# Kernel optimization log

Hardware: AMD Instinct MI355X
Metric: run time of the kernel (lower is better)

The kernel has to match this reference:

```python
import jax, jax.numpy as jnp
import numpy as np

B, S, D = 2, 8192, 1024
H, HD, FD = 16, 64, 256

def setup_inputs() -> dict:
    key = jax.random.key(0)
    ks = jax.random.split(key, 6)
    sc = 1.0 / np.sqrt(D)
    return {
        "hidden_states": jax.random.normal(ks[0], (B, S, D), jnp.float32),
        "Wq": jax.random.normal(ks[1], (D, D), jnp.float32) * sc,
        "Wk": jax.random.normal(ks[2], (D, D), jnp.float32) * sc,
        "Wv": jax.random.normal(ks[3], (D, D), jnp.float32) * sc,
        "Wo": jax.random.normal(ks[4], (D, D), jnp.float32) * sc,
        "Wf": jax.random.normal(ks[5], (FD, HD), jnp.float32) * (1.0 / np.sqrt(HD)),
    }

def reference(hidden_states, Wq, Wk, Wv, Wo, Wf):
    b, s, _ = hidden_states.shape
    # projections (torch Linear: x @ W.T), split heads -> (b, s, h, hd)
    q = (hidden_states @ Wq.T).reshape(b, s, H, HD)
    k = (hidden_states @ Wk.T).reshape(b, s, H, HD)
    v = (hidden_states @ Wv.T).reshape(b, s, H, HD)
    # elu+1 feature map -> (b, s, h, f)
    qf = jax.nn.elu(q @ Wf.T) + 1.0
    kf = jax.nn.elu(k @ Wf.T) + 1.0
    # global kv summary: (b, h, f, d)
    kv = jnp.einsum('bshf,bshd->bhfd', kf, v)
    out = jnp.einsum('bshf,bhfd->bshd', qf, kv)
    k_sum = kf.sum(axis=1)                       # (b, h, f)
    norm = jnp.einsum('bshf,bhf->bsh', qf, k_sum)[..., None] + 1e-6
    out = (out / norm).reshape(b, s, D)
    return out @ Wo.T
```

## Files before the change

kernel.cpp:

```cpp
#include <hip/hip_runtime.h>
#include <stdint.h>

typedef __bf16 bf16_t;
typedef __attribute__((ext_vector_type(8))) __bf16 bfv8;
typedef __attribute__((ext_vector_type(4))) __bf16 bfv4;
typedef __attribute__((ext_vector_type(4))) float f32x4;

constexpr int BATCH = 2, SEQ = 8192, DIM = 1024, NH = 16, HDIM = 64, FDIM = 256;
constexpr int MROWS = BATCH * SEQ;
constexpr int NCHUNK = 16;
constexpr int KV_NIT = (SEQ / NCHUNK) / 32;
constexpr int KVP_CH = 32 * 256 * 68;

__device__ __forceinline__ f32x4 mfma_bf16(bfv8 a, bfv8 b, f32x4 c) {
  return __builtin_amdgcn_mfma_f32_16x16x32_bf16(a, b, c, 0, 0, 0);
}

__device__ __forceinline__ void gload_lds16(const bf16_t* g, bf16_t* lds) {
  auto const* gp = reinterpret_cast<const __attribute__((address_space(1))) uint32_t*>(
      reinterpret_cast<uintptr_t>(g));
  auto* lp = reinterpret_cast<__attribute__((address_space(3))) uint32_t*>(
      reinterpret_cast<uintptr_t>(lds));
  __builtin_amdgcn_global_load_lds(gp, lp, 16, 0, 0);
}

__device__ __forceinline__ void stage128x64(const bf16_t* g_base, int k0,
                                            bf16_t* lds, int wid, int lane) {
#pragma unroll
  for (int j = 0; j < 4; ++j) {
    int r0 = (wid * 4 + j) * 8;
    int g_row = r0 + (lane >> 3);
    int g_slot = (lane & 7) ^ (g_row & 7);
    const bf16_t* src = g_base + (size_t)g_row * DIM + k0 + g_slot * 8;
    gload_lds16(src, lds + r0 * 64);
  }
}

__global__ __launch_bounds__(256) void cvt_all(const float* __restrict__ X,
                                               const float* __restrict__ Wq,
                                               const float* __restrict__ Wk,
                                               const float* __restrict__ Wv,
                                               const float* __restrict__ Wo,
                                               const float* __restrict__ Wf,
                                               bf16_t* __restrict__ Xb,
                                               bf16_t* __restrict__ W3,
                                               bf16_t* __restrict__ Wob,
                                               bf16_t* __restrict__ Wfb) {
  int i = blockIdx.x * 256 + threadIdx.x;
  const float* src;
  bf16_t* dst;
  int off;
  if (i < 4194304) {
    src = X; dst = Xb; off = i;
  } else {
    int j = i - 4194304;
    if (j < 786432) {
      int seg = j >> 18;
      off = j & 262143;
      src = (seg == 0) ? Wq : ((seg == 1) ? Wk : Wv);
      dst = W3 + (size_t)seg * 1048576;
    } else if (j < 1048576) {
      off = j - 786432; src = Wo; dst = Wob;
    } else {
      off = j - 1048576; src = Wf; dst = Wfb;
    }
  }
  float4 v = reinterpret_cast<const float4*>(src)[off];
  bfv4 o = {(__bf16)v.x, (__bf16)v.y, (__bf16)v.z, (__bf16)v.w};
  reinterpret_cast<bfv4*>(dst)[off] = o;
}

__global__ __launch_bounds__(256) void gemm_qkv(const bf16_t* __restrict__ A,
                                                const bf16_t* __restrict__ Wall,
                                                bf16_t* __restrict__ Q,
                                                bf16_t* __restrict__ K,
                                                bf16_t* __restrict__ V) {
  __shared__ bf16_t As[128 * 64];
  __shared__ bf16_t Bs[128 * 64];
  int z = blockIdx.z;
  const bf16_t* Wm = Wall + (size_t)z * (DIM * DIM);
  bf16_t* C = (z == 0) ? Q : ((z == 1) ? K : V);
  int lane = threadIdx.x & 63, wid = threadIdx.x >> 6;
  int lr = lane & 15, lg = lane >> 4;
  int wr = wid >> 1, wc = wid & 1;
  int brow = blockIdx.x * 128, bcol = blockIdx.y * 128;
  const bf16_t* Ab = A + (size_t)brow * DIM;
  const bf16_t* Bb = Wm + (size_t)bcol * DIM;
  f32x4 acc[4][4] = {};
  for (int ks = 0; ks < DIM / 64; ++ks) {
    stage128x64(Ab, ks * 64, As, wid, lane);
    stage128x64(Bb, ks * 64, Bs, wid, lane);
    __syncthreads();
#pragma unroll
    for (int kk = 0; kk < 2; ++kk) {
      bfv8 af[4], bg[4];
#pragma unroll
      for (int t = 0; t < 4; ++t) {
        int ar = wr * 64 + t * 16 + lr;
        af[t] = *reinterpret_cast<const bfv8*>(&As[ar * 64 + (((kk * 4 + lg) ^ (ar & 7)) * 8)]);
        int br = wc * 64 + t * 16 + lr;
        bg[t] = *reinterpret_cast<const bfv8*>(&Bs[br * 64 + (((kk * 4 + lg) ^ (br & 7)) * 8)]);
      }
#pragma unroll
      for (int i = 0; i < 4; ++i)
#pragma unroll
        for (int j = 0; j < 4; ++j) acc[i][j] = mfma_bf16(af[i], bg[j], acc[i][j]);
    }
    __syncthreads();
  }
#pragma unroll
  for (int i = 0; i < 4; ++i) {
    int r = brow + wr * 64 + i * 16 + lg * 4;
#pragma unroll
    for (int j = 0; j < 4; ++j) {
      int c = bcol + wc * 64 + j * 16 + lr;
#pragma unroll
      for (int q = 0; q < 4; ++q) C[(size_t)(r + q) * DIM + c] = (__bf16)acc[i][j][q];
    }
  }
}

__global__ __launch_bounds__(256) void gemm_final(const bf16_t* __restrict__ A,
                                                  const bf16_t* __restrict__ W,
                                                  float* __restrict__ C) {
  __shared__ bf16_t As[128 * 64];
  __shared__ bf16_t Bs[128 * 64];
  int lane = threadIdx.x & 63, wid = threadIdx.x >> 6;
  int lr = lane & 15, lg = lane >> 4;
  int wr = wid >> 1, wc = wid & 1;
  int brow = blockIdx.x * 128, bcol = blockIdx.y * 128;
  const bf16_t* Ab = A + (size_t)brow * DIM;
  const bf16_t* Bb = W + (size_t)bcol * DIM;
  f32x4 acc[4][4] = {};
  for (int ks = 0; ks < DIM / 64; ++ks) {
    stage128x64(Ab, ks * 64, As, wid, lane);
    stage128x64(Bb, ks * 64, Bs, wid, lane);
    __syncthreads();
#pragma unroll
    for (int kk = 0; kk < 2; ++kk) {
      bfv8 af[4], bg[4];
#pragma unroll
      for (int t = 0; t < 4; ++t) {
        int ar = wr * 64 + t * 16 + lr;
        af[t] = *reinterpret_cast<const bfv8*>(&As[ar * 64 + (((kk * 4 + lg) ^ (ar & 7)) * 8)]);
        int br = wc * 64 + t * 16 + lr;
        bg[t] = *reinterpret_cast<const bfv8*>(&Bs[br * 64 + (((kk * 4 + lg) ^ (br & 7)) * 8)]);
      }
#pragma unroll
      for (int i = 0; i < 4; ++i)
#pragma unroll
        for (int j = 0; j < 4; ++j) acc[i][j] = mfma_bf16(af[i], bg[j], acc[i][j]);
    }
    __syncthreads();
  }
#pragma unroll
  for (int i = 0; i < 4; ++i) {
    int r = brow + wr * 64 + i * 16 + lg * 4;
#pragma unroll
    for (int j = 0; j < 4; ++j) {
      int c = bcol + wc * 64 + j * 16 + lr;
#pragma unroll
      for (int q = 0; q < 4; ++q) C[(size_t)(r + q) * DIM + c] = acc[i][j][q];
    }
  }
}

__global__ __launch_bounds__(256, 2) void kv_fused(const bf16_t* __restrict__ Kb,
                                                   const bf16_t* __restrict__ Vb,
                                                   const bf16_t* __restrict__ Wf,
                                                   float* __restrict__ kv_part) {
  __shared__ bf16_t kf_lds[4][64 * 36];
  __shared__ bf16_t vt[4][80 * 36];
  int chunk = blockIdx.x, bh = blockIdx.y;
  int b = bh >> 4, h = bh & 15;
  int lane = threadIdx.x & 63, wid = threadIdx.x >> 6;
  int lr = lane & 15, lg = lane >> 4;
  int f0 = wid * 64;
  for (int i = lane; i < 16 * 36; i += 64) {
    int n = i / 36, s = i - n * 36;
    vt[wid][(64 + n) * 36 + s] = (n == 0) ? (__bf16)1.0f : (__bf16)0.0f;
  }
  bfv8 wf[4][2];
#pragma unroll
  for (int ft = 0; ft < 4; ++ft)
#pragma unroll
    for (int kk = 0; kk < 2; ++kk)
      wf[ft][kk] = *reinterpret_cast<const bfv8*>(Wf + (size_t)(f0 + ft * 16 + lr) * HDIM + kk * 32 + lg * 8);
  const bf16_t* Kbase = Kb + (size_t)b * SEQ * DIM + h * HDIM;
  const bf16_t* Vbase = Vb + (size_t)b * SEQ * DIM + h * HDIM;
  int s0 = chunk * (SEQ / NCHUNK);

  bfv8 krgA[2][2], krgB[2][2];
#pragma unroll
  for (int st = 0; st < 2; ++st)
#pragma unroll
    for (int kk = 0; kk < 2; ++kk)
      krgA[st][kk] = *reinterpret_cast<const bfv8*>(Kbase + (size_t)(s0 + st * 16 + lr) * DIM + kk * 32 + lg * 8);

  f32x4 acc[4][5] = {};

  auto STEP = [&](int it, bfv8(&krgC)[2][2], bfv8(&krgN)[2][2]) __attribute__((always_inline)) {
    int sb = s0 + it * 32;
    bfv8 vv[4];
#pragma unroll
    for (int rep = 0; rep < 4; ++rep) {
      int idx = rep * 64 + lane;
      vv[rep] = *reinterpret_cast<const bfv8*>(Vbase + (size_t)(sb + (idx >> 3)) * DIM + (idx & 7) * 8);
    }
    if (it + 1 < KV_NIT) {
#pragma unroll
      for (int st = 0; st < 2; ++st)
#pragma unroll
        for (int kk = 0; kk < 2; ++kk)
          krgN[st][kk] = *reinterpret_cast<const bfv8*>(Kbase + (size_t)(sb + 32 + st * 16 + lr) * DIM + kk * 32 + lg * 8);
    }
    f32x4 ckf[4][2] = {};
#pragma unroll
    for (int ft = 0; ft < 4; ++ft)
#pragma unroll
      for (int st = 0; st < 2; ++st)
#pragma unroll
        for (int kk = 0; kk < 2; ++kk) ckf[ft][st] = mfma_bf16(wf[ft][kk], krgC[st][kk], ckf[ft][st]);
#pragma unroll
    for (int rep = 0; rep < 4; ++rep) {
      int idx = rep * 64 + lane;
#pragma unroll
      for (int j = 0; j < 8; ++j) vt[wid][((idx & 7) * 8 + j) * 36 + (idx >> 3)] = vv[rep][j];
    }
#pragma unroll
    for (int ft = 0; ft < 4; ++ft)
#pragma unroll
      for (int st = 0; st < 2; ++st)
#pragma unroll
        for (int q = 0; q < 4; ++q) {
          float x = ckf[ft][st][q];
          x = (x > 0.0f) ? (x + 1.0f) : __expf(x);
          kf_lds[wid][(ft * 16 + lg * 4 + q) * 36 + st * 16 + lr] = (__bf16)x;
        }
    bfv8 af[4], bg[5];
#pragma unroll
    for (int ft = 0; ft < 4; ++ft)
      af[ft] = *reinterpret_cast<const bfv8*>(&kf_lds[wid][(ft * 16 + lr) * 36 + lg * 8]);
#pragma unroll
    for (int nt = 0; nt < 5; ++nt)
      bg[nt] = *reinterpret_cast<const bfv8*>(&vt[wid][(nt * 16 + lr) * 36 + lg * 8]);
#pragma unroll
    for (int ft = 0; ft < 4; ++ft)
#pragma unroll
      for (int nt = 0; nt < 5; ++nt) acc[ft][nt] = mfma_bf16(af[ft], bg[nt], acc[ft][nt]);
  };

  for (int it2 = 0; it2 < KV_NIT; it2 += 2) {
    STEP(it2, krgA, krgB);
    STEP(it2 + 1, krgB, krgA);
  }

  float* outb = kv_part + ((size_t)chunk * 32 + bh) * (FDIM * 68);
#pragma unroll
  for (int ft = 0; ft < 4; ++ft)
#pragma unroll
    for (int q = 0; q < 4; ++q) {
      int f = f0 + ft * 16 + lg * 4 + q;
#pragma unroll
      for (int nt = 0; nt < 4; ++nt)
        outb[(size_t)f * 68 + nt * 16 + lr] = acc[ft][nt][q];
      if (lr < 4) outb[(size_t)f * 68 + 64 + lr] = acc[ft][4][q];
    }
}

__global__ __launch_bounds__(256) void kv_reduce(const float* __restrict__ part,
                                                 bf16_t* __restrict__ kvT) {
  int i = blockIdx.x * 256 + threadIdx.x;
  if (i < KVP_CH) {
    int n = i % 68;
    int t = i / 68;
    int f = t & 255, bh = t >> 8;
    float s = 0.0f;
#pragma unroll
    for (int c = 0; c < NCHUNK; ++c) s += part[(size_t)c * KVP_CH + i];
    int fs = ((((f >> 3) ^ (n & 7)) << 3) | (f & 7));
    kvT[((size_t)bh * 80 + n) * FDIM + fs] = (__bf16)s;
  } else {
    int j = i - KVP_CH;
    int f = j & 255;
    int t = j >> 8;
    int n = 68 + t % 12, bh = t / 12;
    kvT[((size_t)bh * 80 + n) * FDIM + f] = (__bf16)0.0f;
  }
}

__global__ __launch_bounds__(256) void attn_fused(const bf16_t* __restrict__ Qb,
                                                  const bf16_t* __restrict__ Wf,
                                                  const bf16_t* __restrict__ kvT,
                                                  bf16_t* __restrict__ outp) {
  __shared__ bf16_t qf_lds[64 * 264];
  __shared__ bf16_t kv_lds[80 * 256];
  int rb = blockIdx.x, h = blockIdx.y;
  int row0 = rb * 64;
  int bh = (row0 >> 13) * NH + h;
  int lane = threadIdx.x & 63, wid = threadIdx.x >> 6;
  int lr = lane & 15, lg = lane >> 4;
  int f0 = wid * 64;
  const bf16_t* kvTb = kvT + (size_t)bh * 80 * FDIM;
#pragma unroll
  for (int i = 0; i < 10; ++i) {
    int sbase = wid * 640 + i * 64;
    gload_lds16(kvTb + (size_t)(sbase + lane) * 8, kv_lds + sbase * 8);
  }
  bfv8 qa[4][2], wfb[4][2];
#pragma unroll
  for (int t = 0; t < 4; ++t)
#pragma unroll
    for (int kk = 0; kk < 2; ++kk) {
      qa[t][kk] = *reinterpret_cast<const bfv8*>(Qb + (size_t)(row0 + t * 16 + lr) * DIM + h * HDIM + kk * 32 + lg * 8);
      wfb[t][kk] = *reinterpret_cast<const bfv8*>(Wf + (size_t)(f0 + t * 16 + lr) * HDIM + kk * 32 + lg * 8);
    }
  f32x4 cq[4][4] = {};
#pragma unroll
  for (int rt = 0; rt < 4; ++rt)
#pragma unroll
    for (int ft = 0; ft < 4; ++ft)
#pragma unroll
      for (int kk = 0; kk < 2; ++kk) cq[rt][ft] = mfma_bf16(qa[rt][kk], wfb[ft][kk], cq[rt][ft]);
#pragma unroll
  for (int rt = 0; rt < 4; ++rt)
#pragma unroll
    for (int ft = 0; ft < 4; ++ft)
#pragma unroll
      for (int q = 0; q < 4; ++q) {
        float x = cq[rt][ft][q];
        x = (x > 0.0f) ? (x + 1.0f) : __expf(x);
        qf_lds[(size_t)(rt * 16 + lg * 4 + q) * 264 + f0 + ft * 16 + lr] = (__bf16)x;
      }
  __syncthreads();
  f32x4 acc[5] = {};
#pragma unroll
  for (int ks = 0; ks < 8; ++ks) {
    bfv8 a = *reinterpret_cast<const bfv8*>(&qf_lds[(size_t)(wid * 16 + lr) * 264 + ks * 32 + lg * 8]);
#pragma unroll
    for (int nt = 0; nt < 5; ++nt) {
      bfv8 bg = *reinterpret_cast<const bfv8*>(
          &kv_lds[(size_t)(nt * 16 + lr) * 256 + (((ks * 4 + lg) ^ (lr & 7)) * 8)]);
      acc[nt] = mfma_bf16(a, bg, acc[nt]);
    }
  }
  __syncthreads();
#pragma unroll
  for (int q = 0; q < 4; ++q) {
    float nrm = __shfl(acc[4][q], (lane & 48)) + 1e-6f;
    int row = wid * 16 + lg * 4 + q;
#pragma unroll
    for (int nt = 0; nt < 4; ++nt)
      qf_lds[(size_t)row * 264 + nt * 16 + lr] = (__bf16)(acc[nt][q] / nrm);
  }
  __syncthreads();
#pragma unroll
  for (int rep = 0; rep < 2; ++rep) {
    int id = rep * 256 + threadIdx.x;
    int row = id >> 3, c8 = id & 7;
    bfv8 v = *reinterpret_cast<const bfv8*>(&qf_lds[(size_t)row * 264 + c8 * 8]);
    *reinterpret_cast<bfv8*>(&outp[(size_t)(row0 + row) * DIM + h * HDIM + c8 * 8]) = v;
  }
}

extern "C" void kernel_launch(void* const* d_in, const int* in_sizes, int n_in,
                              void* d_out, int out_size, void* d_ws, size_t ws_size,
                              hipStream_t stream) {
  const float* X  = (const float*)d_in[0];
  const float* Wq = (const float*)d_in[1];
  const float* Wk = (const float*)d_in[2];
  const float* Wv = (const float*)d_in[3];
  const float* Wo = (const float*)d_in[4];
  const float* Wf = (const float*)d_in[5];
  float* out = (float*)d_out;
  char* ws = (char*)d_ws;
  const size_t MB = 1ull << 20;
  if (ws_size < 75 * MB) return;

  bf16_t* Xb  = (bf16_t*)(ws + 0 * MB);
  bf16_t* W3  = (bf16_t*)(ws + 32 * MB);
  bf16_t* Qb  = (bf16_t*)(ws + 38 * MB);
  bf16_t* Wob = (bf16_t*)(ws + 70 * MB);
  bf16_t* Wfb = (bf16_t*)(ws + 72 * MB);
  bf16_t* kvT = (bf16_t*)(ws + 73 * MB);
  float* kv_part = (float*)(ws + 0 * MB);
  bf16_t* outp = (bf16_t*)(ws + 0 * MB);
  bf16_t* Kb = (bf16_t*)d_out;
  bf16_t* Vb = Kb + (size_t)MROWS * DIM;

  cvt_all<<<20496, 256, 0, stream>>>(X, Wq, Wk, Wv, Wo, Wf, Xb, W3, Wob, Wfb);

  gemm_qkv<<<dim3(128, 8, 3), 256, 0, stream>>>(Xb, W3, Qb, Kb, Vb);
  kv_fused<<<dim3(NCHUNK, 32), 256, 0, stream>>>(Kb, Vb, Wfb, kv_part);
  kv_reduce<<<2560, 256, 0, stream>>>(kv_part, kvT);
  attn_fused<<<dim3(256, NH), 256, 0, stream>>>(Qb, Wfb, kvT, outp);
  gemm_final<<<dim3(128, 8), 256, 0, stream>>>(outp, Wob, out);
}
```

Measured before the change: 301.0 us.

## Double-buffer LDS tiles in QKV and output projection GEMMs

New measurement: 283.2 us. 5.9% less time.

```diff
diff --git a/kernel.cpp b/kernel.cpp
--- a/kernel.cpp
+++ b/kernel.cpp
@@ -75,8 +75,8 @@
                                                 bf16_t* __restrict__ Q,
                                                 bf16_t* __restrict__ K,
                                                 bf16_t* __restrict__ V) {
-  __shared__ bf16_t As[128 * 64];
-  __shared__ bf16_t Bs[128 * 64];
+  __shared__ bf16_t As[2][128 * 64];
+  __shared__ bf16_t Bs[2][128 * 64];
   int z = blockIdx.z;
   const bf16_t* Wm = Wall + (size_t)z * (DIM * DIM);
   bf16_t* C = (z == 0) ? Q : ((z == 1) ? K : V);
@@ -87,27 +87,42 @@
   const bf16_t* Ab = A + (size_t)brow * DIM;
   const bf16_t* Bb = Wm + (size_t)bcol * DIM;
   f32x4 acc[4][4] = {};
-  for (int ks = 0; ks < DIM / 64; ++ks) {
-    stage128x64(Ab, ks * 64, As, wid, lane);
-    stage128x64(Bb, ks * 64, Bs, wid, lane);
-    __syncthreads();
+
+  stage128x64(Ab, 0, As[0], wid, lane);
+  stage128x64(Bb, 0, Bs[0], wid, lane);
+  asm volatile("s_waitcnt vmcnt(0)" ::: "memory");
+  __builtin_amdgcn_s_barrier();
+
+  auto TILE = [&](const bf16_t* Acur, const bf16_t* Bcur, bf16_t* Anext, bf16_t* Bnext,
+                  int knext) __attribute__((always_inline)) {
+    if (knext < DIM) {
+      stage128x64(Ab, knext, Anext, wid, lane);
+      stage128x64(Bb, knext, Bnext, wid, lane);
+    }
 #pragma unroll
     for (int kk = 0; kk < 2; ++kk) {
       bfv8 af[4], bg[4];
 #pragma unroll
       for (int t = 0; t < 4; ++t) {
         int ar = wr * 64 + t * 16 + lr;
-        af[t] = *reinterpret_cast<const bfv8*>(&As[ar * 64 + (((kk * 4 + lg) ^ (ar & 7)) * 8)]);
+        af[t] = *reinterpret_cast<const bfv8*>(&Acur[ar * 64 + (((kk * 4 + lg) ^ (ar & 7)) * 8)]);
         int br = wc * 64 + t * 16 + lr;
-        bg[t] = *reinterpret_cast<const bfv8*>(&Bs[br * 64 + (((kk * 4 + lg) ^ (br & 7)) * 8)]);
+        bg[t] = *reinterpret_cast<const bfv8*>(&Bcur[br * 64 + (((kk * 4 + lg) ^ (br & 7)) * 8)]);
       }
 #pragma unroll
       for (int i = 0; i < 4; ++i)
 #pragma unroll
         for (int j = 0; j < 4; ++j) acc[i][j] = mfma_bf16(af[i], bg[j], acc[i][j]);
     }
-    __syncthreads();
-  }
+    asm volatile("s_waitcnt vmcnt(0)" ::: "memory");
+    __builtin_amdgcn_s_barrier();
+  };
+
+  for (int ks = 0; ks < DIM / 64; ks += 2) {
+    TILE(As[0], Bs[0], As[1], Bs[1], (ks + 1) * 64);
+    TILE(As[1], Bs[1], As[0], Bs[0], (ks + 2) * 64);
+  }
+
 #pragma unroll
   for (int i = 0; i < 4; ++i) {
     int r = brow + wr * 64 + i * 16 + lg * 4;
@@ -123,8 +138,8 @@
 __global__ __launch_bounds__(256) void gemm_final(const bf16_t* __restrict__ A,
                                                   const bf16_t* __restrict__ W,
                                                   float* __restrict__ C) {
-  __shared__ bf16_t As[128 * 64];
-  __shared__ bf16_t Bs[128 * 64];
+  __shared__ bf16_t As[2][128 * 64];
+  __shared__ bf16_t Bs[2][128 * 64];
   int lane = threadIdx.x & 63, wid = threadIdx.x >> 6;
   int lr = lane & 15, lg = lane >> 4;
   int wr = wid >> 1, wc = wid & 1;
@@ -132,27 +147,42 @@
   const bf16_t* Ab = A + (size_t)brow * DIM;
   const bf16_t* Bb = W + (size_t)bcol * DIM;
   f32x4 acc[4][4] = {};
-  for (int ks = 0; ks < DIM / 64; ++ks) {
-    stage128x64(Ab, ks * 64, As, wid, lane);
-    stage128x64(Bb, ks * 64, Bs, wid, lane);
-    __syncthreads();
+
+  stage128x64(Ab, 0, As[0], wid, lane);
+  stage128x64(Bb, 0, Bs[0], wid, lane);
+  asm volatile("s_waitcnt vmcnt(0)" ::: "memory");
+  __builtin_amdgcn_s_barrier();
+
+  auto TILE = [&](const bf16_t* Acur, const bf16_t* Bcur, bf16_t* Anext, bf16_t* Bnext,
+                  int knext) __attribute__((always_inline)) {
+    if (knext < DIM) {
+      stage128x64(Ab, knext, Anext, wid, lane);
+      stage128x64(Bb, knext, Bnext, wid, lane);
+    }
 #pragma unroll
     for (int kk = 0; kk < 2; ++kk) {
       bfv8 af[4], bg[4];
 #pragma unroll
       for (int t = 0; t < 4; ++t) {
         int ar = wr * 64 + t * 16 + lr;
-        af[t] = *reinterpret_cast<const bfv8*>(&As[ar * 64 + (((kk * 4 + lg) ^ (ar & 7)) * 8)]);
+        af[t] = *reinterpret_cast<const bfv8*>(&Acur[ar * 64 + (((kk * 4 + lg) ^ (ar & 7)) * 8)]);
         int br = wc * 64 + t * 16 + lr;
-        bg[t] = *reinterpret_cast<const bfv8*>(&Bs[br * 64 + (((kk * 4 + lg) ^ (br & 7)) * 8)]);
+        bg[t] = *reinterpret_cast<const bfv8*>(&Bcur[br * 64 + (((kk * 4 + lg) ^ (br & 7)) * 8)]);
       }
 #pragma unroll
       for (int i = 0; i < 4; ++i)
 #pragma unroll
         for (int j = 0; j < 4; ++j) acc[i][j] = mfma_bf16(af[i], bg[j], acc[i][j]);
     }
-    __syncthreads();
-  }
+    asm volatile("s_waitcnt vmcnt(0)" ::: "memory");
+    __builtin_amdgcn_s_barrier();
+  };
+
+  for (int ks = 0; ks < DIM / 64; ks += 2) {
+    TILE(As[0], Bs[0], As[1], Bs[1], (ks + 1) * 64);
+    TILE(As[1], Bs[1], As[0], Bs[0], (ks + 2) * 64);
+  }
+
 #pragma unroll
   for (int i = 0; i < 4; ++i) {
     int r = brow + wr * 64 + i * 16 + lg * 4;
```
